# Kernel tuning notes

Measured on AMD Instinct MI355X. Metric: run time of the kernel, lower is better.

## Reference

```python
import jax, jax.numpy as jnp
import numpy as np

STRIDE = 1  # stride3x3 init arg


def sparsemax(z):
    """Sparsemax along last axis (Martins & Astudillo 2016)."""
    K = z.shape[-1]
    zs = -jnp.sort(-z, axis=-1)                     # sorted descending
    cum = jnp.cumsum(zs, axis=-1)
    ks = jnp.arange(1, K + 1, dtype=z.dtype)
    support = (1 + ks * zs) > cum                   # [.., K] bool
    k_z = jnp.sum(support, axis=-1, keepdims=True)  # support size, int
    cum_k = jnp.take_along_axis(cum, k_z - 1, axis=-1)
    tau = (cum_k - 1) / k_z.astype(z.dtype)
    return jnp.maximum(z - tau, 0)


def setup_inputs() -> dict:
    key = jax.random.key(0)
    k1, k2, k3, k4 = jax.random.split(key, 4)
    B, Cin, Cout, H, W, K = 64, 512, 512, 28, 28, 8
    x = jax.random.normal(k1, (B, Cin, H, W), dtype=jnp.float32)
    gate_w = jax.random.normal(k2, (K, Cin), dtype=jnp.float32) * 0.02   # nn.Linear weight
    gate_b = jax.random.normal(k3, (K,), dtype=jnp.float32) * 0.02       # nn.Linear bias
    expert_w = jax.random.normal(k4, (K, Cout, Cin), dtype=jnp.float32) * 0.02  # K conv1x1 kernels (bias-free)
    return {"x": x, "gate_w": gate_w, "gate_b": gate_b, "expert_w": expert_w}


def reference(x, gate_w, gate_b, expert_w):
    # gate: sparsemax(Linear(mean_pool(x)))
    pooled = x.mean(axis=(2, 3))                         # [B, Cin]
    g = sparsemax(pooled @ gate_w.T + gate_b)            # [B, K], many exact zeros
    # sum_k g[b,k] * conv1x1_k(x) == conv1x1 with per-sample combined weight
    xs = x[:, :, ::STRIDE, ::STRIDE]                     # 1x1 conv with stride = subsample
    w_eff = jnp.einsum('bk,koi->boi', g, expert_w)       # [B, Cout, Cin]
    out = jnp.einsum('boi,bihw->bohw', w_eff, xs)        # [B, Cout, H', W']
    return out
```

## Files before the change

kernel.cpp:

```cpp
#include <hip/hip_runtime.h>

#define NB 64
#define CIN 512
#define COUT 512
#define HW 784
#define KEXP 8

typedef __attribute__((ext_vector_type(8))) short bf16x8;
typedef __attribute__((ext_vector_type(4))) float f32x4;

typedef const __attribute__((address_space(1))) unsigned int GU32;
typedef __attribute__((address_space(3))) unsigned int LU32;

__device__ __forceinline__ unsigned f2bf1(float f) {
  unsigned u = __builtin_bit_cast(unsigned, f);
  return (u + 0x7FFFu + ((u >> 16) & 1u)) >> 16;
}
__device__ __forceinline__ unsigned f2bf2(float lo, float hi) {
  return f2bf1(lo) | (f2bf1(hi) << 16);
}

__global__ __launch_bounds__(256) void xtpool_kernel(const float* __restrict__ x,
                                                     uint4* __restrict__ xt,
                                                     float* __restrict__ parts) {
  __shared__ float tile[32][116];
  int id = blockIdx.x;
  int kk = id & 15, bn = id >> 4;
  int b = bn / 7, nb = bn - b * 7;
  const float* xsrc = x + (size_t)b * (CIN * HW) + (size_t)kk * 32 * HW + nb * 112;
  uint4* dst = xt + (size_t)id * 448;
  int t = threadIdx.x;

  #pragma unroll
  for (int i = 0; i < 4; ++i) {
    int u = t + i * 256;
    if (u < 896) {
      int r = u / 28, c4 = u - r * 28;
      float4 v = ((const float4*)(xsrc + (size_t)r * HW))[c4];
      *(float4*)&tile[r][c4 * 4] = v;
    }
  }
  __syncthreads();

  {
    int pr = t >> 3, pp = t & 7;
    float s = 0.f;
    #pragma unroll
    for (int i = 0; i < 14; ++i) s += tile[pr][pp * 14 + i];
    s += __shfl_xor(s, 1); s += __shfl_xor(s, 2); s += __shfl_xor(s, 4);
    if (pp == 0) parts[((size_t)nb * NB + b) * CIN + kk * 32 + pr] = s;
  }

  {
    int k0 = t / 112, c0 = t - k0 * 112;
    uint4 pk;
    pk.x = f2bf2(tile[k0 * 8 + 0][c0], tile[k0 * 8 + 1][c0]);
    pk.y = f2bf2(tile[k0 * 8 + 2][c0], tile[k0 * 8 + 3][c0]);
    pk.z = f2bf2(tile[k0 * 8 + 4][c0], tile[k0 * 8 + 5][c0]);
    pk.w = f2bf2(tile[k0 * 8 + 6][c0], tile[k0 * 8 + 7][c0]);
    dst[t] = pk;
  }
  if (t < 192) {
    int t2 = 256 + t, k1 = t2 / 112, c1 = t2 - k1 * 112;
    uint4 pk;
    pk.x = f2bf2(tile[k1 * 8 + 0][c1], tile[k1 * 8 + 1][c1]);
    pk.y = f2bf2(tile[k1 * 8 + 2][c1], tile[k1 * 8 + 3][c1]);
    pk.z = f2bf2(tile[k1 * 8 + 4][c1], tile[k1 * 8 + 5][c1]);
    pk.w = f2bf2(tile[k1 * 8 + 6][c1], tile[k1 * 8 + 7][c1]);
    dst[256 + t] = pk;
  }
}

__global__ __launch_bounds__(256) void gate_kernel(const float* __restrict__ parts,
                                                   const float* __restrict__ gw,
                                                   const float* __restrict__ gb,
                                                   float* __restrict__ g) {
  __shared__ float red[4][KEXP];
  int b = blockIdx.x;
  int t = threadIdx.x;
  int lane = t & 63, w = t >> 6;

  float p0 = 0.f, p1 = 0.f;
  #pragma unroll
  for (int q = 0; q < 7; ++q) {
    const float* pr = parts + (size_t)q * (NB * CIN) + b * CIN;
    p0 += pr[t];
    p1 += pr[t + 256];
  }
  float zk[KEXP];
  #pragma unroll
  for (int k = 0; k < KEXP; ++k)
    zk[k] = p0 * gw[k * CIN + t] + p1 * gw[k * CIN + t + 256];

  #pragma unroll
  for (int k = 0; k < KEXP; ++k) {
    float s = zk[k];
    #pragma unroll
    for (int off = 32; off; off >>= 1) s += __shfl_down(s, off);
    if (lane == 0) red[w][k] = s;
  }
  __syncthreads();

  if (t == 0) {
    float z[8], zs[8];
    #pragma unroll
    for (int j = 0; j < 8; ++j) {
      z[j] = (red[0][j] + red[1][j] + red[2][j] + red[3][j]) * (1.0f / 784.0f) + gb[j];
      zs[j] = z[j];
    }
    #pragma unroll
    for (int a = 1; a < 8; ++a) {
      float v = zs[a]; int j = a;
      while (j > 0 && zs[j - 1] < v) { zs[j] = zs[j - 1]; --j; }
      zs[j] = v;
    }
    float cums[8]; float csum = 0.f;
    #pragma unroll
    for (int j = 0; j < 8; ++j) { csum += zs[j]; cums[j] = csum; }
    int kz = 0;
    #pragma unroll
    for (int j = 0; j < 8; ++j)
      if (1.0f + (float)(j + 1) * zs[j] > cums[j]) kz = j + 1;
    float tau = (cums[kz - 1] - 1.0f) / (float)kz;
    #pragma unroll
    for (int j = 0; j < 8; ++j) g[b * 8 + j] = fmaxf(z[j] - tau, 0.0f);
  }
}

__global__ __launch_bounds__(256) void weff_kernel(const float* __restrict__ E,
                                                   const float* __restrict__ g,
                                                   uint4* __restrict__ wt) {
  __shared__ float gs[NB * KEXP];
  int t = threadIdx.x;
  ((float2*)gs)[t] = ((const float2*)g)[t];
  int o = blockIdx.x * 16 + (t & 15);
  int i = blockIdx.y * 128 + (t >> 4) * 8;
  int b0 = blockIdx.z * 32;
  float e[8][8];
  #pragma unroll
  for (int k = 0; k < 8; ++k) {
    const float4* p = (const float4*)(E + (size_t)k * (COUT * CIN) + (size_t)o * CIN + i);
    float4 a = p[0], c = p[1];
    e[k][0] = a.x; e[k][1] = a.y; e[k][2] = a.z; e[k][3] = a.w;
    e[k][4] = c.x; e[k][5] = c.y; e[k][6] = c.z; e[k][7] = c.w;
  }
  __syncthreads();
  int base = ((o >> 8) * 16 + (i >> 5)) * 1024 + ((i >> 3) & 3) * 256 + (o & 255);
  for (int b = b0; b < b0 + 32; ++b) {
    float acc[8] = {0, 0, 0, 0, 0, 0, 0, 0};
    #pragma unroll
    for (int k = 0; k < 8; ++k) {
      float gv = gs[b * 8 + k];
      #pragma unroll
      for (int j = 0; j < 8; ++j) acc[j] += gv * e[k][j];
    }
    uint4 pk;
    pk.x = f2bf2(acc[0], acc[1]); pk.y = f2bf2(acc[2], acc[3]);
    pk.z = f2bf2(acc[4], acc[5]); pk.w = f2bf2(acc[6], acc[7]);
    wt[(size_t)base + (size_t)b * 32768] = pk;
  }
}

#define VMCNT(n) asm volatile("s_waitcnt vmcnt(" #n ")" ::: "memory")
__global__ __launch_bounds__(512) void gemm_kernel(const uint4* __restrict__ weff,
                                                   const uint4* __restrict__ xt,
                                                   float* __restrict__ out) {
  __shared__ uint4 ldsA[3][1024];
  __shared__ uint4 ldsB[3][448];
  int id = blockIdx.x;
  int xcd = id & 7, s = id >> 3;
  int bloc = s / 14, inner = s - bloc * 14;
  int b = xcd * 8 + bloc;
  int mb = inner & 1, nb = inner >> 1;

  int t = threadIdx.x;
  int lane = t & 63, w = t >> 6;
  int l15 = lane & 15, l4 = lane >> 4;

  const uint4* asrc = weff + (size_t)b * 32768 + (size_t)mb * 16384;
  const uint4* bsrc = xt + (size_t)(b * 7 + nb) * 7168;

  int s1 = w * 64 + lane, fs1 = s1 ^ ((s1 >> 3) & 7);

  f32x4 acc[2][7] = {};

#define STAGE(buf, kk)                                                          \
  do {                                                                          \
    _Pragma("unroll")                                                           \
    for (int it = 0; it < 2; ++it)                                              \
      __builtin_amdgcn_global_load_lds((GU32*)(asrc + (kk) * 1024 + it * 512 + t), \
                                       (LU32*)(&ldsA[buf][it * 512 + w * 64]), 16, 0, 0); \
    if (w < 7)                                                                  \
      __builtin_amdgcn_global_load_lds((GU32*)(bsrc + (kk) * 448 + fs1),        \
                                       (LU32*)(&ldsB[buf][w * 64]), 16, 0, 0);  \
  } while (0)

  STAGE(0, 0);
  STAGE(1, 1);

  int cur = 0;
  for (int kk = 0; kk < 16; ++kk) {
    if (kk < 15) {
      if (w < 7) VMCNT(3); else VMCNT(2);
    } else {
      VMCNT(0);
    }
    __builtin_amdgcn_s_barrier();
    __builtin_amdgcn_sched_barrier(0);

    if (kk < 14) {
      int nxt = cur + 2; if (nxt >= 3) nxt -= 3;
      STAGE(nxt, kk + 2);
    }

    bf16x8 af[2];
    #pragma unroll
    for (int m = 0; m < 2; ++m)
      af[m] = *(const bf16x8*)&ldsA[cur][l4 * 256 + w * 32 + m * 16 + l15];
    #pragma unroll
    for (int u = 0; u < 7; ++u) {
      int un = l4 * 112 + u * 16 + l15;
      bf16x8 bf = *(const bf16x8*)&ldsB[cur][un ^ ((un >> 3) & 7)];
      #pragma unroll
      for (int m = 0; m < 2; ++m)
        acc[m][u] = __builtin_amdgcn_mfma_f32_16x16x32_bf16(af[m], bf, acc[m][u], 0, 0, 0);
    }

    if (++cur >= 3) cur = 0;
  }
#undef STAGE

  int orow0 = mb * 256 + w * 32 + l4 * 4;
  int col = nb * 112 + l15;
  #pragma unroll
  for (int m = 0; m < 2; ++m) {
    #pragma unroll
    for (int u = 0; u < 7; ++u) {
      float* op = out + ((size_t)b * COUT + orow0 + m * 16) * HW + col + u * 16;
      #pragma unroll
      for (int r = 0; r < 4; ++r) op[(size_t)r * HW] = acc[m][u][r];
    }
  }
}

extern "C" void kernel_launch(void* const* d_in, const int* in_sizes, int n_in,
                              void* d_out, int out_size, void* d_ws, size_t ws_size,
                              hipStream_t stream) {
  const float* x        = (const float*)d_in[0];
  const float* gate_w   = (const float*)d_in[1];
  const float* gate_b   = (const float*)d_in[2];
  const float* expert_w = (const float*)d_in[3];
  float* out = (float*)d_out;

  char* ws = (char*)d_ws;
  uint4* weff   = (uint4*)ws;
  uint4* xt     = (uint4*)(ws + 33554432);
  float* parts  = (float*)(ws + 33554432 + 51380224);
  float* g      = (float*)(ws + 33554432 + 51380224 + 917504);

  xtpool_kernel<<<7168, 256, 0, stream>>>(x, xt, parts);
  gate_kernel<<<NB, 256, 0, stream>>>(parts, gate_w, gate_b, g);
  weff_kernel<<<dim3(32, 4, 2), 256, 0, stream>>>(expert_w, g, weff);
  gemm_kernel<<<896, 512, 0, stream>>>(weff, xt, out);
}
```

Baseline: 93.06 us.

## Load A fragments directly into registers instead of staging through LDS

New measurement: 100.9 us. +8.5%, slower.

```diff
diff --git a/kernel.cpp b/kernel.cpp
--- a/kernel.cpp
+++ b/kernel.cpp
@@ -165,7 +165,6 @@
 __global__ __launch_bounds__(512) void gemm_kernel(const uint4* __restrict__ weff,
                                                    const uint4* __restrict__ xt,
                                                    float* __restrict__ out) {
-  __shared__ uint4 ldsA[3][1024];
   __shared__ uint4 ldsB[3][448];
   int id = blockIdx.x;
   int xcd = id & 7, s = id >> 3;
@@ -177,58 +176,56 @@
   int lane = t & 63, w = t >> 6;
   int l15 = lane & 15, l4 = lane >> 4;
 
-  const uint4* asrc = weff + (size_t)b * 32768 + (size_t)mb * 16384;
+  const uint4* asrc = weff + (size_t)b * 32768 + (size_t)mb * 16384
+                      + l4 * 256 + w * 32 + l15;
   const uint4* bsrc = xt + (size_t)(b * 7 + nb) * 7168;
 
   int s1 = w * 64 + lane, fs1 = s1 ^ ((s1 >> 3) & 7);
 
   f32x4 acc[2][7] = {};
-
-#define STAGE(buf, kk)                                                          \
-  do {                                                                          \
-    _Pragma("unroll")                                                           \
-    for (int it = 0; it < 2; ++it)                                              \
-      __builtin_amdgcn_global_load_lds((GU32*)(asrc + (kk) * 1024 + it * 512 + t), \
-                                       (LU32*)(&ldsA[buf][it * 512 + w * 64]), 16, 0, 0); \
-    if (w < 7)                                                                  \
-      __builtin_amdgcn_global_load_lds((GU32*)(bsrc + (kk) * 448 + fs1),        \
-                                       (LU32*)(&ldsB[buf][w * 64]), 16, 0, 0);  \
-  } while (0)
-
-  STAGE(0, 0);
-  STAGE(1, 1);
-
-  int cur = 0;
+  uint4 a[3][2];
+
+  #pragma unroll
+  for (int p = 0; p < 2; ++p) {
+    if (w < 7)
+      __builtin_amdgcn_global_load_lds((GU32*)(bsrc + p * 448 + fs1),
+                                       (LU32*)(&ldsB[p][s1]), 16, 0, 0);
+    a[p][0] = asrc[p * 1024];
+    a[p][1] = asrc[p * 1024 + 16];
+  }
+  if (w < 7) { VMCNT(3); } else { VMCNT(2); }
+
+  #pragma unroll
   for (int kk = 0; kk < 16; ++kk) {
-    if (kk < 15) {
-      if (w < 7) VMCNT(3); else VMCNT(2);
-    } else {
-      VMCNT(0);
-    }
     __builtin_amdgcn_s_barrier();
     __builtin_amdgcn_sched_barrier(0);
 
     if (kk < 14) {
-      int nxt = cur + 2; if (nxt >= 3) nxt -= 3;
-      STAGE(nxt, kk + 2);
-    }
-
-    bf16x8 af[2];
-    #pragma unroll
-    for (int m = 0; m < 2; ++m)
-      af[m] = *(const bf16x8*)&ldsA[cur][l4 * 256 + w * 32 + m * 16 + l15];
+      if (w < 7)
+        __builtin_amdgcn_global_load_lds((GU32*)(bsrc + (kk + 2) * 448 + fs1),
+                                         (LU32*)(&ldsB[(kk + 2) % 3][s1]), 16, 0, 0);
+      a[(kk + 2) % 3][0] = asrc[(kk + 2) * 1024];
+      a[(kk + 2) % 3][1] = asrc[(kk + 2) * 1024 + 16];
+    }
+    __builtin_amdgcn_sched_barrier(0);
+
+    bf16x8 af0 = __builtin_bit_cast(bf16x8, a[kk % 3][0]);
+    bf16x8 af1 = __builtin_bit_cast(bf16x8, a[kk % 3][1]);
     #pragma unroll
     for (int u = 0; u < 7; ++u) {
       int un = l4 * 112 + u * 16 + l15;
-      bf16x8 bf = *(const bf16x8*)&ldsB[cur][un ^ ((un >> 3) & 7)];
-      #pragma unroll
-      for (int m = 0; m < 2; ++m)
-        acc[m][u] = __builtin_amdgcn_mfma_f32_16x16x32_bf16(af[m], bf, acc[m][u], 0, 0, 0);
-    }
-
-    if (++cur >= 3) cur = 0;
-  }
-#undef STAGE
+      bf16x8 bf = *(const bf16x8*)&ldsB[kk % 3][un ^ ((un >> 3) & 7)];
+      acc[0][u] = __builtin_amdgcn_mfma_f32_16x16x32_bf16(af0, bf, acc[0][u], 0, 0, 0);
+      acc[1][u] = __builtin_amdgcn_mfma_f32_16x16x32_bf16(af1, bf, acc[1][u], 0, 0, 0);
+    }
+
+    if (kk < 14) {
+      if (w < 7) { VMCNT(3); } else { VMCNT(2); }
+    } else if (kk == 14) {
+      VMCNT(0);
+    }
+    __builtin_amdgcn_sched_barrier(0);
+  }
 
   int orow0 = mb * 256 + w * 32 + l4 * 4;
   int col = nb * 112 + l15;
```
